# Performance work log

Measured on AMD Instinct MI355X. Metric: run time of the kernel, lower is better.

The kernel has to match this reference:

```python
import jax, jax.numpy as jnp
import numpy as np

N = 200000   # total nodes across batched graphs
E = 800000   # directed edges (grid graph, avg degree ~4)
G = 8        # number of graphs in the batch
IN_DIM, INTER_DIM, OUT_DIM, LAYER_NUM = 2, 128, 64, 4


def setup_inputs() -> dict:
    key = jax.random.key(0)
    ks = jax.random.split(key, 10)
    x = jax.random.normal(ks[0], (N, IN_DIM), jnp.float32)
    edge_index = jax.random.randint(ks[1], (2, E), 0, N, dtype=jnp.int32)
    batch = jnp.sort(jax.random.randint(ks[2], (N,), 0, G, dtype=jnp.int32))

    def glorot(k, fan_in, fan_out):
        s = (2.0 / (fan_in + fan_out)) ** 0.5
        return jax.random.normal(k, (fan_in, fan_out), jnp.float32) * s

    W_in = glorot(ks[3], IN_DIM, INTER_DIM)
    b_in = jnp.zeros((INTER_DIM,), jnp.float32)
    W_hidden = jnp.stack([glorot(jax.random.fold_in(ks[4], i), INTER_DIM, INTER_DIM)
                          for i in range(LAYER_NUM)])
    b_hidden = jnp.zeros((LAYER_NUM, INTER_DIM), jnp.float32)
    W_out = glorot(ks[5], INTER_DIM, OUT_DIM)
    b_out = jnp.zeros((OUT_DIM,), jnp.float32)
    return {"x": x, "edge_index": edge_index, "batch": batch,
            "W_in": W_in, "b_in": b_in, "W_hidden": W_hidden,
            "b_hidden": b_hidden, "W_out": W_out, "b_out": b_out}


def reference(x, edge_index, batch, W_in, b_in, W_hidden, b_hidden, W_out, b_out):
    num_nodes = x.shape[0]
    loops = jnp.arange(num_nodes, dtype=edge_index.dtype)
    # PyG GCNConv: add self loops, symmetric degree normalization
    src = jnp.concatenate([edge_index[0], loops])
    dst = jnp.concatenate([edge_index[1], loops])
    deg = jax.ops.segment_sum(jnp.ones_like(src, x.dtype), dst, num_segments=num_nodes)
    dinv = jnp.where(deg > 0, jax.lax.rsqrt(jnp.maximum(deg, 1.0)), 0.0)
    norm = dinv[src] * dinv[dst]  # [E+N]

    def gcn_conv(h, W, b):
        m = h @ W                                  # [N, F'] dense transform
        msg = norm[:, None] * m[src]               # gather + scale
        out = jax.ops.segment_sum(msg, dst, num_segments=num_nodes)  # scatter-add
        return out + b

    h = gcn_conv(x, W_in, b_in)
    for i in range(W_hidden.shape[0]):
        h = jax.nn.relu(gcn_conv(h, W_hidden[i], b_hidden[i]))
    h = gcn_conv(h, W_out, b_out)

    # global mean pool over batch assignment, then sigmoid
    sums = jax.ops.segment_sum(h, batch, num_segments=G)
    cnts = jax.ops.segment_sum(jnp.ones((num_nodes,), h.dtype), batch, num_segments=G)
    return jax.nn.sigmoid(sums / jnp.maximum(cnts, 1.0)[:, None])
```

## Files before the change

### kernel.cpp

```cpp
#include <hip/hip_runtime.h>
#include <math.h>

#define INTER 128
#define OUTD  64
#define SCAN_T 256
#define SCAN_E 1024
#define NBIN  256
#define PNB2  512
#define NSLOT 64

using bf16x8 = __attribute__((ext_vector_type(8))) short;
using f32x4  = __attribute__((ext_vector_type(4))) float;

static __device__ __forceinline__ unsigned short f2bf(float f) {
    unsigned int u = __float_as_uint(f);
    u += 0x7fffu + ((u >> 16) & 1u);
    return (unsigned short)(u >> 16);
}
static __device__ __forceinline__ unsigned int pk2(float a, float b) {
    return (unsigned int)f2bf(a) | ((unsigned int)f2bf(b) << 16);
}
static __device__ __forceinline__ float bflo(unsigned int u) { return __uint_as_float(u << 16); }
static __device__ __forceinline__ float bfhi(unsigned int u) { return __uint_as_float(u & 0xffff0000u); }

static __device__ __forceinline__ void fma8(float* a, float w, uint4 v) {
    a[0] = fmaf(w, bflo(v.x), a[0]); a[1] = fmaf(w, bfhi(v.x), a[1]);
    a[2] = fmaf(w, bflo(v.y), a[2]); a[3] = fmaf(w, bfhi(v.y), a[3]);
    a[4] = fmaf(w, bflo(v.z), a[4]); a[5] = fmaf(w, bfhi(v.z), a[5]);
    a[6] = fmaf(w, bflo(v.w), a[6]); a[7] = fmaf(w, bfhi(v.w), a[7]);
}
static __device__ __forceinline__ void seed8(float* a, float sn, uint4 v) {
    a[0] = sn * bflo(v.x); a[1] = sn * bfhi(v.x);
    a[2] = sn * bflo(v.y); a[3] = sn * bfhi(v.y);
    a[4] = sn * bflo(v.z); a[5] = sn * bfhi(v.z);
    a[6] = sn * bflo(v.w); a[7] = sn * bfhi(v.w);
}

__global__ void count_k(const int* __restrict__ dst, int* __restrict__ cnt, int E) {
    int e = blockIdx.x * 256 + threadIdx.x;
    if (e < E) atomicAdd(&cnt[dst[e]], 1);
}

__global__ void scan_block(const int* __restrict__ in, int* __restrict__ out,
                           int* __restrict__ bsums, int n) {
    __shared__ int sh[SCAN_T];
    int base = blockIdx.x * SCAN_E;
    int t = threadIdx.x;
    int v[4];
    int s = 0;
#pragma unroll
    for (int i = 0; i < 4; i++) {
        int idx = base + t * 4 + i;
        v[i] = (idx < n) ? in[idx] : 0;
        s += v[i];
    }
    sh[t] = s;
    __syncthreads();
    for (int off = 1; off < SCAN_T; off <<= 1) {
        int x = (t >= off) ? sh[t - off] : 0;
        __syncthreads();
        sh[t] += x;
        __syncthreads();
    }
    int excl = (t == 0) ? 0 : sh[t - 1];
    if (bsums && t == SCAN_T - 1) bsums[blockIdx.x] = sh[t];
#pragma unroll
    for (int i = 0; i < 4; i++) {
        int idx = base + t * 4 + i;
        if (idx < n) out[idx] = excl;
        excl += v[i];
    }
}

__global__ void scan_add(int* __restrict__ out, const int* __restrict__ bsums, int n, int total) {
    int idx = blockIdx.x * SCAN_E + threadIdx.x * 4;
    int add = bsums[blockIdx.x];
#pragma unroll
    for (int i = 0; i < 4; i++) {
        int j = idx + i;
        if (j < n) out[j] += add;
    }
    if (blockIdx.x == 0 && threadIdx.x == 0) out[n] = total;
}

__global__ void scatter_k(const int* __restrict__ src, const int* __restrict__ dst,
                          const int* __restrict__ rs, int* __restrict__ cursor,
                          const float* __restrict__ dinv,
                          int2* __restrict__ cw, int E) {
    int e = blockIdx.x * 256 + threadIdx.x;
    if (e >= E) return;
    int s = src[e], d = dst[e];
    int pos = rs[d] + atomicAdd(&cursor[d], 1);
    cw[pos] = make_int2(s, __float_as_int(dinv[s] * dinv[d]));
}

__global__ __launch_bounds__(256) void prep2_k(const int* __restrict__ cnt,
                                               const int* __restrict__ batch,
                                               float* __restrict__ dinv,
                                               int* __restrict__ blockhist,
                                               int* __restrict__ gstart,
                                               int N, int G, int nblk) {
    __shared__ int hist[NBIN];
    int t = threadIdx.x;
    if (t < NBIN) hist[t] = 0;
    __syncthreads();
    int i = blockIdx.x * 256 + t;
    if (i < N) {
        int d = cnt[i];
        dinv[i] = rsqrtf((float)(d + 1));
        int b = batch[i];
        atomicAdd(&hist[b * 32 + min(d, 31)], 1);
        int prev = (i == 0) ? -1 : batch[i - 1];
        for (int g2 = prev + 1; g2 <= b; g2++) gstart[g2] = i;
        if (i == N - 1) for (int g2 = b + 1; g2 <= G; g2++) gstart[g2] = N;
    }
    __syncthreads();
    if (t < NBIN) blockhist[t * nblk + blockIdx.x] = hist[t];
}

__global__ __launch_bounds__(256) void dorder3_k(const int* __restrict__ cnt,
                                                 const int* __restrict__ batch,
                                                 const int* __restrict__ rs,
                                                 const float* __restrict__ dinv,
                                                 const int* __restrict__ offs,
                                                 int4* __restrict__ srt,
                                                 int N, int nblk) {
    __shared__ int cur[NBIN];
    int t = threadIdx.x;
    if (t < NBIN) cur[t] = 0;
    __syncthreads();
    int i = blockIdx.x * 256 + t;
    if (i >= N) return;
    int key = batch[i] * 32 + min(cnt[i], 31);
    int r = atomicAdd(&cur[key], 1);
    int p = offs[key * nblk + blockIdx.x] + r;
    srt[p] = make_int4(i, rs[i], rs[i + 1], __float_as_int(dinv[i]));
}

__global__ void wprep_h(const float* __restrict__ W, unsigned short* __restrict__ Wt, int L) {
    int tid = blockIdx.x * 256 + threadIdx.x;
    if (tid >= L * INTER * INTER) return;
    int l = tid / (INTER * INTER);
    int r = tid % (INTER * INTER);
    int n = r / INTER, k = r % INTER;
    Wt[tid] = f2bf(W[(size_t)l * INTER * INTER + (size_t)k * INTER + n]);
}

__global__ __launch_bounds__(256) void agg_in_k(const float* __restrict__ x,
                                                const int* __restrict__ rs,
                                                const int2* __restrict__ cw,
                                                const float* __restrict__ dinv,
                                                const float* __restrict__ Wi,
                                                const float* __restrict__ bi,
                                                unsigned short* __restrict__ h, int N) {
    __shared__ float2 axs[256];
    int t = threadIdx.x;
    int i = blockIdx.x * 256 + t;
    float a0 = 0.f, a1 = 0.f;
    if (i < N) {
        float di = dinv[i];
        float sn = di * di;
        float2 xv = ((const float2*)x)[i];
        a0 = sn * xv.x; a1 = sn * xv.y;
        int e0 = rs[i], e1 = rs[i + 1];
        for (int k = e0; k < e1; k += 2) {
            int2 c0 = cw[k];
            int2 c1 = (k + 1 < e1) ? cw[k + 1] : make_int2(0, 0);
            float2 x0 = ((const float2*)x)[c0.x];
            float2 x1 = ((const float2*)x)[c1.x];
            float w0 = __int_as_float(c0.y), w1 = __int_as_float(c1.y);
            a0 = fmaf(w0, x0.x, a0); a1 = fmaf(w0, x0.y, a1);
            a0 = fmaf(w1, x1.x, a0); a1 = fmaf(w1, x1.y, a1);
        }
    }
    axs[t] = make_float2(a0, a1);
    __syncthreads();
    int base = blockIdx.x * 256;
#pragma unroll
    for (int p = 0; p < 16; p++) {
        int nl = p * 16 + (t >> 4);
        int nb = base + nl;
        if (nb < N) {
            int j0 = (t & 15) * 8;
            float2 a = axs[nl];
            float4 wa0 = *(const float4*)&Wi[j0];       float4 wa1 = *(const float4*)&Wi[j0 + 4];
            float4 wb0 = *(const float4*)&Wi[128 + j0]; float4 wb1 = *(const float4*)&Wi[128 + j0 + 4];
            float4 bb0 = *(const float4*)&bi[j0];       float4 bb1 = *(const float4*)&bi[j0 + 4];
            float h0 = fmaf(a.x, wa0.x, fmaf(a.y, wb0.x, bb0.x));
            float h1 = fmaf(a.x, wa0.y, fmaf(a.y, wb0.y, bb0.y));
            float h2 = fmaf(a.x, wa0.z, fmaf(a.y, wb0.z, bb0.z));
            float h3 = fmaf(a.x, wa0.w, fmaf(a.y, wb0.w, bb0.w));
            float h4 = fmaf(a.x, wa1.x, fmaf(a.y, wb1.x, bb1.x));
            float h5 = fmaf(a.x, wa1.y, fmaf(a.y, wb1.y, bb1.y));
            float h6 = fmaf(a.x, wa1.z, fmaf(a.y, wb1.z, bb1.z));
            float h7 = fmaf(a.x, wa1.w, fmaf(a.y, wb1.w, bb1.w));
            *(uint4*)(h + (size_t)nb * 128 + j0) =
                make_uint4(pk2(h0, h1), pk2(h2, h3), pk2(h4, h5), pk2(h6, h7));
        }
    }
}

__global__ __launch_bounds__(256) void fused_hidden7(
    const unsigned short* __restrict__ Hin,
    const int2* __restrict__ cw,
    const int4* __restrict__ srt,
    const unsigned short* __restrict__ Wt,
    const float* __restrict__ bias,
    unsigned short* __restrict__ Hout, int N)
{
    __shared__ __align__(16) unsigned short T[32][136];
    __shared__ int nodeid[32];
    const int t = threadIdx.x;
    const int q = t & 15;
    const int gi = t >> 4;
    const int sA = blockIdx.x * 32 + gi;
    const int sB = sA + 16;
    int4 dA = (sA < N) ? srt[sA] : make_int4(-1, 0, 0, 0);
    int4 dB = (sB < N) ? srt[sB] : make_int4(-1, 0, 0, 0);
    if (q == 0) {
        nodeid[gi]      = dA.x;
        nodeid[gi + 16] = dB.x;
    }

    float accA[8] = {0,0,0,0,0,0,0,0}, accB[8] = {0,0,0,0,0,0,0,0};
    int kA = 0, eA = 0, kB = 0, eB = 0;
    if (dA.x >= 0) {
        float dv = __int_as_float(dA.w);
        seed8(accA, dv * dv, *(const uint4*)(Hin + (size_t)dA.x * 128 + q * 8));
        kA = dA.y; eA = dA.z;
    }
    if (dB.x >= 0) {
        float dv = __int_as_float(dB.w);
        seed8(accB, dv * dv, *(const uint4*)(Hin + (size_t)dB.x * 128 + q * 8));
        kB = dB.y; eB = dB.z;
    }

    while (kA < eA || kB < eB) {
        int2 cA0 = (kA     < eA) ? cw[kA]     : make_int2(0, 0);
        int2 cA1 = (kA + 1 < eA) ? cw[kA + 1] : make_int2(0, 0);
        int2 cA2 = (kA + 2 < eA) ? cw[kA + 2] : make_int2(0, 0);
        int2 cA3 = (kA + 3 < eA) ? cw[kA + 3] : make_int2(0, 0);
        int2 cB0 = (kB     < eB) ? cw[kB]     : make_int2(0, 0);
        int2 cB1 = (kB + 1 < eB) ? cw[kB + 1] : make_int2(0, 0);
        int2 cB2 = (kB + 2 < eB) ? cw[kB + 2] : make_int2(0, 0);
        int2 cB3 = (kB + 3 < eB) ? cw[kB + 3] : make_int2(0, 0);
        uint4 vA0 = *(const uint4*)(Hin + (size_t)cA0.x * 128 + q * 8);
        uint4 vA1 = *(const uint4*)(Hin + (size_t)cA1.x * 128 + q * 8);
        uint4 vA2 = *(const uint4*)(Hin + (size_t)cA2.x * 128 + q * 8);
        uint4 vA3 = *(const uint4*)(Hin + (size_t)cA3.x * 128 + q * 8);
        uint4 vB0 = *(const uint4*)(Hin + (size_t)cB0.x * 128 + q * 8);
        uint4 vB1 = *(const uint4*)(Hin + (size_t)cB1.x * 128 + q * 8);
        uint4 vB2 = *(const uint4*)(Hin + (size_t)cB2.x * 128 + q * 8);
        uint4 vB3 = *(const uint4*)(Hin + (size_t)cB3.x * 128 + q * 8);
        fma8(accA, __int_as_float(cA0.y), vA0);
        fma8(accA, __int_as_float(cA1.y), vA1);
        fma8(accA, __int_as_float(cA2.y), vA2);
        fma8(accA, __int_as_float(cA3.y), vA3);
        fma8(accB, __int_as_float(cB0.y), vB0);
        fma8(accB, __int_as_float(cB1.y), vB1);
        fma8(accB, __int_as_float(cB2.y), vB2);
        fma8(accB, __int_as_float(cB3.y), vB3);
        kA += 4; kB += 4;
    }

    {
        uint4 oA = make_uint4(pk2(accA[0], accA[1]), pk2(accA[2], accA[3]),
                              pk2(accA[4], accA[5]), pk2(accA[6], accA[7]));
        uint4 oB = make_uint4(pk2(accB[0], accB[1]), pk2(accB[2], accB[3]),
                              pk2(accB[4], accB[5]), pk2(accB[6], accB[7]));
        *(uint4*)&T[gi][q * 8] = oA;
        *(uint4*)&T[gi + 16][q * 8] = oB;
    }
    __syncthreads();

    const int wv = t >> 6;
    const int lane = t & 63;
    const int r15 = lane & 15;
    const int kg = lane >> 4;

    bf16x8 bfr[2][4];
#pragma unroll
    for (int nc = 0; nc < 2; nc++)
#pragma unroll
        for (int ks = 0; ks < 4; ks++)
            bfr[nc][ks] = *(const bf16x8*)&T[nc * 16 + r15][kg * 8 + ks * 32];

    f32x4 acc[2][2];
#pragma unroll
    for (int nc = 0; nc < 2; nc++)
#pragma unroll
        for (int c = 0; c < 2; c++) acc[nc][c] = (f32x4){0.f, 0.f, 0.f, 0.f};

#pragma unroll
    for (int c = 0; c < 2; c++) {
        const unsigned short* wrow = Wt + (size_t)(wv * 32 + c * 16 + r15) * 128 + kg * 8;
#pragma unroll
        for (int ks = 0; ks < 4; ks++) {
            bf16x8 afr = *(const bf16x8*)(wrow + ks * 32);
            acc[0][c] = __builtin_amdgcn_mfma_f32_16x16x32_bf16(afr, bfr[0][ks], acc[0][c], 0, 0, 0);
            acc[1][c] = __builtin_amdgcn_mfma_f32_16x16x32_bf16(afr, bfr[1][ks], acc[1][c], 0, 0, 0);
        }
    }

#pragma unroll
    for (int nc = 0; nc < 2; nc++) {
        const int node = nodeid[nc * 16 + r15];
        if (node >= 0) {
#pragma unroll
            for (int c = 0; c < 2; c++) {
                int col = wv * 32 + c * 16 + kg * 4;
                float4 bv = *(const float4*)(bias + col);
                float v0 = fmaxf(acc[nc][c][0] + bv.x, 0.f);
                float v1 = fmaxf(acc[nc][c][1] + bv.y, 0.f);
                float v2 = fmaxf(acc[nc][c][2] + bv.z, 0.f);
                float v3 = fmaxf(acc[nc][c][3] + bv.w, 0.f);
                *(uint2*)(Hout + (size_t)node * 128 + col) = make_uint2(pk2(v0, v1), pk2(v2, v3));
            }
        }
    }
}

__global__ void colsum_k(const int* __restrict__ src, const int* __restrict__ dst,
                         const int* __restrict__ batch, const float* __restrict__ dinv,
                         float* __restrict__ colsum, int N, int E) {
    int e = blockIdx.x * 256 + threadIdx.x;
    if (e < E) {
        int s = src[e], d = dst[e];
        atomicAdd(&colsum[(size_t)batch[d] * N + s], dinv[s] * dinv[d]);
    } else if (e < E + N) {
        int i = e - E;
        float di = dinv[i];
        atomicAdd(&colsum[(size_t)batch[i] * N + i], di * di);
    }
}

__global__ __launch_bounds__(256) void wpool128_k(const unsigned short* __restrict__ hin,
                                                  const float* __restrict__ colsum,
                                                  float* __restrict__ gsum, int N) {
    const int t = threadIdx.x;
    const int wv = t >> 6;
    const int lane = t & 63;
    const int f16 = lane & 15;
    const int r = lane >> 4;
    const int g0 = wv * 2;
    float acc[2][8];
#pragma unroll
    for (int a = 0; a < 2; a++)
#pragma unroll
        for (int b = 0; b < 8; b++) acc[a][b] = 0.f;

    int base = blockIdx.x * PNB2;
    int end = min(base + PNB2, N);
    for (int j = base + r; j < end; j += 4) {
        uint4 v = *(const uint4*)(hin + (size_t)j * 128 + f16 * 8);
        float c0 = colsum[(size_t)g0 * N + j];
        float c1 = colsum[(size_t)(g0 + 1) * N + j];
        float xv[8] = {bflo(v.x), bfhi(v.x), bflo(v.y), bfhi(v.y),
                       bflo(v.z), bfhi(v.z), bflo(v.w), bfhi(v.w)};
#pragma unroll
        for (int b = 0; b < 8; b++) {
            acc[0][b] = fmaf(c0, xv[b], acc[0][b]);
            acc[1][b] = fmaf(c1, xv[b], acc[1][b]);
        }
    }
#pragma unroll
    for (int a = 0; a < 2; a++)
#pragma unroll
        for (int b = 0; b < 8; b++) {
            float v = acc[a][b];
            v += __shfl_xor(v, 16, 64);
            v += __shfl_xor(v, 32, 64);
            acc[a][b] = v;
        }
    if (r == 0) {
        int slot = blockIdx.x & (NSLOT - 1);
        float* dstp = gsum + ((size_t)slot * 8 + g0) * 128 + f16 * 8;
#pragma unroll
        for (int a = 0; a < 2; a++)
#pragma unroll
            for (int b = 0; b < 8; b++)
                atomicAdd(&dstp[(size_t)a * 128 + b], acc[a][b]);
    }
}

__global__ void final6_k(const float* __restrict__ gsum, const int* __restrict__ gstart,
                         const float* __restrict__ W_out, const float* __restrict__ b_out,
                         float* __restrict__ out) {
    __shared__ float sg[8][128];
    int t = threadIdx.x;
    for (int i = t; i < 1024; i += 512) {
        int g = i >> 7, k = i & 127;
        float s = 0.f;
        for (int sl = 0; sl < NSLOT; sl++) s += gsum[((size_t)sl * 8 + g) * 128 + k];
        sg[g][k] = s;
    }
    __syncthreads();
    int g = t / 64, f = t % 64;
    float dot = 0.f;
    for (int k = 0; k < 128; k++) dot = fmaf(sg[g][k], W_out[k * 64 + f], dot);
    int c = gstart[g + 1] - gstart[g];
    float v = dot / (float)max(c, 1) + b_out[f];
    out[g * 64 + f] = 1.f / (1.f + expf(-v));
}

extern "C" void kernel_launch(void* const* d_in, const int* in_sizes, int n_in,
                              void* d_out, int out_size, void* d_ws, size_t ws_size,
                              hipStream_t stream) {
    const float* x     = (const float*)d_in[0];
    const int*   ei    = (const int*)d_in[1];
    const int*   batch = (const int*)d_in[2];
    const float* W_in  = (const float*)d_in[3];
    const float* b_in  = (const float*)d_in[4];
    const float* W_h   = (const float*)d_in[5];
    const float* b_h   = (const float*)d_in[6];
    const float* W_out = (const float*)d_in[7];
    const float* b_out = (const float*)d_in[8];

    const int N = in_sizes[2];
    const int E = in_sizes[1] / 2;
    const int L = in_sizes[5] / (INTER * INTER);
    const int G = 8;
    const int* src = ei;
    const int* dst = ei + E;
    const int nblk = (N + 255) / 256;
    const int nbh = NBIN * nblk;

    char* ws = (char*)d_ws;
    size_t off = 0;
    auto alloc = [&](size_t bytes) -> void* {
        void* p = ws + off;
        off += (bytes + 255) & ~(size_t)255;
        return p;
    };
    int*   cnt    = (int*)alloc((size_t)N * 4);
    int*   cursor = (int*)alloc((size_t)N * 4);
    int*   rs     = (int*)alloc((size_t)(N + 1) * 4);
    int*   bsums  = (int*)alloc(4096);
    float* dinv   = (float*)alloc((size_t)N * 4);
    int2*  cw     = (int2*)alloc((size_t)E * 8);
    unsigned short* h   = (unsigned short*)alloc((size_t)N * INTER * 2);
    unsigned short* h2  = (unsigned short*)alloc((size_t)N * INTER * 2);
    unsigned short* Wht = (unsigned short*)alloc((size_t)L * INTER * INTER * 2);
    float* colsum = (float*)alloc((size_t)8 * N * 4);
    float* gsum   = (float*)alloc((size_t)NSLOT * 8 * 128 * 4);
    int*   gstart = (int*)alloc((G + 1) * 4);
    int*   bh     = (int*)alloc((size_t)(nbh + 1) * 4);
    int4*  srt    = (int4*)alloc((size_t)N * 16);
    (void)ws_size; (void)n_in;

    hipMemsetAsync(cnt, 0, (size_t)N * 8, stream);
    hipMemsetAsync(colsum, 0, (size_t)8 * N * 4, stream);
    hipMemsetAsync(gsum, 0, (size_t)NSLOT * 8 * 128 * 4, stream);

    count_k<<<(E + 255) / 256, 256, 0, stream>>>(dst, cnt, E);
    int nsb = (N + SCAN_E - 1) / SCAN_E;
    scan_block<<<nsb, SCAN_T, 0, stream>>>(cnt, rs, bsums, N);
    scan_block<<<1, SCAN_T, 0, stream>>>(bsums, bsums, nullptr, nsb);
    scan_add<<<nsb, SCAN_T, 0, stream>>>(rs, bsums, N, E);
    prep2_k<<<nblk, 256, 0, stream>>>(cnt, batch, dinv, bh, gstart, N, G, nblk);
    scatter_k<<<(E + 255) / 256, 256, 0, stream>>>(src, dst, rs, cursor, dinv, cw, E);
    colsum_k<<<(E + N + 255) / 256, 256, 0, stream>>>(src, dst, batch, dinv, colsum, N, E);

    int nsb2 = (nbh + SCAN_E - 1) / SCAN_E;
    scan_block<<<nsb2, SCAN_T, 0, stream>>>(bh, bh, bsums, nbh);
    scan_block<<<1, SCAN_T, 0, stream>>>(bsums, bsums, nullptr, nsb2);
    scan_add<<<nsb2, SCAN_T, 0, stream>>>(bh, bsums, nbh, N);
    dorder3_k<<<nblk, 256, 0, stream>>>(cnt, batch, rs, dinv, bh, srt, N, nblk);

    wprep_h<<<(L * INTER * INTER + 255) / 256, 256, 0, stream>>>(W_h, Wht, L);

    agg_in_k<<<nblk, 256, 0, stream>>>(x, rs, cw, dinv, W_in, b_in, h, N);

    unsigned short* hin = h;
    unsigned short* hout = h2;
    for (int l = 0; l < L; l++) {
        fused_hidden7<<<(N + 31) / 32, 256, 0, stream>>>(
            hin, cw, srt, Wht + (size_t)l * INTER * INTER, b_h + (size_t)l * INTER, hout, N);
        unsigned short* tmp = hin; hin = hout; hout = tmp;
    }

    wpool128_k<<<(N + PNB2 - 1) / PNB2, 256, 0, stream>>>(hin, colsum, gsum, N);
    final6_k<<<1, 512, 0, stream>>>(gsum, gstart, W_out, b_out, (float*)d_out);
}
```

Baseline: 521.6 us.

## Use one node per thread-group in hidden layer and fuse scatter with colsum

The hidden-layer kernel now uses 512 threads per block, with each 16-lane group aggregating a single node, unrolled by 8 edges, instead of two interleaved nodes per group. The MFMA stage is split so each of 8 waves produces 16 output columns. Results are staged through shared memory so each node's 256-byte output row is written as one coalesced store. Separately, the CSR scatter and colsum kernels are merged to save a launch and reread inputs once. The tradeoffs are more syncthreads per block, higher register pressure, and per-group load imbalance from the unroll-by-8 padding.

```diff
diff --git a/kernel.cpp b/kernel.cpp
--- a/kernel.cpp
+++ b/kernel.cpp
@@ -83,15 +83,23 @@
     if (blockIdx.x == 0 && threadIdx.x == 0) out[n] = total;
 }
 
-__global__ void scatter_k(const int* __restrict__ src, const int* __restrict__ dst,
-                          const int* __restrict__ rs, int* __restrict__ cursor,
-                          const float* __restrict__ dinv,
-                          int2* __restrict__ cw, int E) {
+__global__ void scatter_cs_k(const int* __restrict__ src, const int* __restrict__ dst,
+                             const int* __restrict__ rs, int* __restrict__ cursor,
+                             const float* __restrict__ dinv, const int* __restrict__ batch,
+                             int2* __restrict__ cw, float* __restrict__ colsum,
+                             int N, int E) {
     int e = blockIdx.x * 256 + threadIdx.x;
-    if (e >= E) return;
-    int s = src[e], d = dst[e];
-    int pos = rs[d] + atomicAdd(&cursor[d], 1);
-    cw[pos] = make_int2(s, __float_as_int(dinv[s] * dinv[d]));
+    if (e < E) {
+        int s = src[e], d = dst[e];
+        float w = dinv[s] * dinv[d];
+        int pos = rs[d] + atomicAdd(&cursor[d], 1);
+        cw[pos] = make_int2(s, __float_as_int(w));
+        atomicAdd(&colsum[(size_t)batch[d] * N + s], w);
+    } else if (e < E + N) {
+        int i = e - E;
+        float di = dinv[i];
+        atomicAdd(&colsum[(size_t)batch[i] * N + i], di * di);
+    }
 }
 
 __global__ __launch_bounds__(256) void prep2_k(const int* __restrict__ cnt,
@@ -200,7 +208,7 @@
     }
 }
 
-__global__ __launch_bounds__(256) void fused_hidden7(
+__global__ __launch_bounds__(512) void fused_hidden9(
     const unsigned short* __restrict__ Hin,
     const int2* __restrict__ cw,
     const int4* __restrict__ srt,
@@ -213,64 +221,34 @@
     const int t = threadIdx.x;
     const int q = t & 15;
     const int gi = t >> 4;
-    const int sA = blockIdx.x * 32 + gi;
-    const int sB = sA + 16;
-    int4 dA = (sA < N) ? srt[sA] : make_int4(-1, 0, 0, 0);
-    int4 dB = (sB < N) ? srt[sB] : make_int4(-1, 0, 0, 0);
-    if (q == 0) {
-        nodeid[gi]      = dA.x;
-        nodeid[gi + 16] = dB.x;
-    }
-
-    float accA[8] = {0,0,0,0,0,0,0,0}, accB[8] = {0,0,0,0,0,0,0,0};
-    int kA = 0, eA = 0, kB = 0, eB = 0;
-    if (dA.x >= 0) {
-        float dv = __int_as_float(dA.w);
-        seed8(accA, dv * dv, *(const uint4*)(Hin + (size_t)dA.x * 128 + q * 8));
-        kA = dA.y; eA = dA.z;
-    }
-    if (dB.x >= 0) {
-        float dv = __int_as_float(dB.w);
-        seed8(accB, dv * dv, *(const uint4*)(Hin + (size_t)dB.x * 128 + q * 8));
-        kB = dB.y; eB = dB.z;
-    }
-
-    while (kA < eA || kB < eB) {
-        int2 cA0 = (kA     < eA) ? cw[kA]     : make_int2(0, 0);
-        int2 cA1 = (kA + 1 < eA) ? cw[kA + 1] : make_int2(0, 0);
-        int2 cA2 = (kA + 2 < eA) ? cw[kA + 2] : make_int2(0, 0);
-        int2 cA3 = (kA + 3 < eA) ? cw[kA + 3] : make_int2(0, 0);
-        int2 cB0 = (kB     < eB) ? cw[kB]     : make_int2(0, 0);
-        int2 cB1 = (kB + 1 < eB) ? cw[kB + 1] : make_int2(0, 0);
-        int2 cB2 = (kB + 2 < eB) ? cw[kB + 2] : make_int2(0, 0);
-        int2 cB3 = (kB + 3 < eB) ? cw[kB + 3] : make_int2(0, 0);
-        uint4 vA0 = *(const uint4*)(Hin + (size_t)cA0.x * 128 + q * 8);
-        uint4 vA1 = *(const uint4*)(Hin + (size_t)cA1.x * 128 + q * 8);
-        uint4 vA2 = *(const uint4*)(Hin + (size_t)cA2.x * 128 + q * 8);
-        uint4 vA3 = *(const uint4*)(Hin + (size_t)cA3.x * 128 + q * 8);
-        uint4 vB0 = *(const uint4*)(Hin + (size_t)cB0.x * 128 + q * 8);
-        uint4 vB1 = *(const uint4*)(Hin + (size_t)cB1.x * 128 + q * 8);
-        uint4 vB2 = *(const uint4*)(Hin + (size_t)cB2.x * 128 + q * 8);
-        uint4 vB3 = *(const uint4*)(Hin + (size_t)cB3.x * 128 + q * 8);
-        fma8(accA, __int_as_float(cA0.y), vA0);
-        fma8(accA, __int_as_float(cA1.y), vA1);
-        fma8(accA, __int_as_float(cA2.y), vA2);
-        fma8(accA, __int_as_float(cA3.y), vA3);
-        fma8(accB, __int_as_float(cB0.y), vB0);
-        fma8(accB, __int_as_float(cB1.y), vB1);
-        fma8(accB, __int_as_float(cB2.y), vB2);
-        fma8(accB, __int_as_float(cB3.y), vB3);
-        kA += 4; kB += 4;
-    }
-
-    {
-        uint4 oA = make_uint4(pk2(accA[0], accA[1]), pk2(accA[2], accA[3]),
-                              pk2(accA[4], accA[5]), pk2(accA[6], accA[7]));
-        uint4 oB = make_uint4(pk2(accB[0], accB[1]), pk2(accB[2], accB[3]),
-                              pk2(accB[4], accB[5]), pk2(accB[6], accB[7]));
-        *(uint4*)&T[gi][q * 8] = oA;
-        *(uint4*)&T[gi + 16][q * 8] = oB;
-    }
+    const int s = blockIdx.x * 32 + gi;
+    int4 d0 = (s < N) ? srt[s] : make_int4(-1, 0, 0, 0);
+    if (q == 0) nodeid[gi] = d0.x;
+
+    float acc[8] = {0,0,0,0,0,0,0,0};
+    int k0 = 0, e0 = 0;
+    if (d0.x >= 0) {
+        float dv = __int_as_float(d0.w);
+        seed8(acc, dv * dv, *(const uint4*)(Hin + (size_t)d0.x * 128 + q * 8));
+        k0 = d0.y; e0 = d0.z;
+    }
+
+    for (int k = k0; k < e0; k += 8) {
+        int2 c[8];
+#pragma unroll
+        for (int u = 0; u < 8; u++)
+            c[u] = (k + u < e0) ? cw[k + u] : make_int2(0, 0);
+        uint4 v[8];
+#pragma unroll
+        for (int u = 0; u < 8; u++)
+            v[u] = *(const uint4*)(Hin + (size_t)c[u].x * 128 + q * 8);
+#pragma unroll
+        for (int u = 0; u < 8; u++)
+            fma8(acc, __int_as_float(c[u].y), v[u]);
+    }
+
+    *(uint4*)&T[gi][q * 8] = make_uint4(pk2(acc[0], acc[1]), pk2(acc[2], acc[3]),
+                                        pk2(acc[4], acc[5]), pk2(acc[6], acc[7]));
     __syncthreads();
 
     const int wv = t >> 6;
@@ -278,59 +256,45 @@
     const int r15 = lane & 15;
     const int kg = lane >> 4;
 
-    bf16x8 bfr[2][4];
-#pragma unroll
-    for (int nc = 0; nc < 2; nc++)
+    bf16x8 wfr[4];
+    {
+        const unsigned short* wrow = Wt + (size_t)(wv * 16 + r15) * 128 + kg * 8;
 #pragma unroll
         for (int ks = 0; ks < 4; ks++)
-            bfr[nc][ks] = *(const bf16x8*)&T[nc * 16 + r15][kg * 8 + ks * 32];
-
-    f32x4 acc[2][2];
-#pragma unroll
-    for (int nc = 0; nc < 2; nc++)
-#pragma unroll
-        for (int c = 0; c < 2; c++) acc[nc][c] = (f32x4){0.f, 0.f, 0.f, 0.f};
-
-#pragma unroll
-    for (int c = 0; c < 2; c++) {
-        const unsigned short* wrow = Wt + (size_t)(wv * 32 + c * 16 + r15) * 128 + kg * 8;
+            wfr[ks] = *(const bf16x8*)(wrow + ks * 32);
+    }
+
+    f32x4 a2[2];
+    a2[0] = (f32x4){0.f, 0.f, 0.f, 0.f};
+    a2[1] = (f32x4){0.f, 0.f, 0.f, 0.f};
+#pragma unroll
+    for (int nc = 0; nc < 2; nc++) {
 #pragma unroll
         for (int ks = 0; ks < 4; ks++) {
-            bf16x8 afr = *(const bf16x8*)(wrow + ks * 32);
-            acc[0][c] = __builtin_amdgcn_mfma_f32_16x16x32_bf16(afr, bfr[0][ks], acc[0][c], 0, 0, 0);
-            acc[1][c] = __builtin_amdgcn_mfma_f32_16x16x32_bf16(afr, bfr[1][ks], acc[1][c], 0, 0, 0);
-        }
-    }
-
-#pragma unroll
-    for (int nc = 0; nc < 2; nc++) {
-        const int node = nodeid[nc * 16 + r15];
-        if (node >= 0) {
-#pragma unroll
-            for (int c = 0; c < 2; c++) {
-                int col = wv * 32 + c * 16 + kg * 4;
-                float4 bv = *(const float4*)(bias + col);
-                float v0 = fmaxf(acc[nc][c][0] + bv.x, 0.f);
-                float v1 = fmaxf(acc[nc][c][1] + bv.y, 0.f);
-                float v2 = fmaxf(acc[nc][c][2] + bv.z, 0.f);
-                float v3 = fmaxf(acc[nc][c][3] + bv.w, 0.f);
-                *(uint2*)(Hout + (size_t)node * 128 + col) = make_uint2(pk2(v0, v1), pk2(v2, v3));
-            }
-        }
-    }
-}
-
-__global__ void colsum_k(const int* __restrict__ src, const int* __restrict__ dst,
-                         const int* __restrict__ batch, const float* __restrict__ dinv,
-                         float* __restrict__ colsum, int N, int E) {
-    int e = blockIdx.x * 256 + threadIdx.x;
-    if (e < E) {
-        int s = src[e], d = dst[e];
-        atomicAdd(&colsum[(size_t)batch[d] * N + s], dinv[s] * dinv[d]);
-    } else if (e < E + N) {
-        int i = e - E;
-        float di = dinv[i];
-        atomicAdd(&colsum[(size_t)batch[i] * N + i], di * di);
+            bf16x8 bfr = *(const bf16x8*)&T[nc * 16 + r15][kg * 8 + ks * 32];
+            a2[nc] = __builtin_amdgcn_mfma_f32_16x16x32_bf16(wfr[ks], bfr, a2[nc], 0, 0, 0);
+        }
+    }
+    __syncthreads();
+
+    {
+        const int col = wv * 16 + kg * 4;
+        const float4 bv = *(const float4*)(bias + col);
+#pragma unroll
+        for (int nc = 0; nc < 2; nc++) {
+            float v0 = fmaxf(a2[nc][0] + bv.x, 0.f);
+            float v1 = fmaxf(a2[nc][1] + bv.y, 0.f);
+            float v2 = fmaxf(a2[nc][2] + bv.z, 0.f);
+            float v3 = fmaxf(a2[nc][3] + bv.w, 0.f);
+            *(uint2*)&T[nc * 16 + r15][col] = make_uint2(pk2(v0, v1), pk2(v2, v3));
+        }
+    }
+    __syncthreads();
+
+    {
+        int node = nodeid[gi];
+        if (node >= 0)
+            *(uint4*)(Hout + (size_t)node * 128 + q * 8) = *(const uint4*)&T[gi][q * 8];
     }
 }
 
@@ -458,8 +422,8 @@
     scan_block<<<1, SCAN_T, 0, stream>>>(bsums, bsums, nullptr, nsb);
     scan_add<<<nsb, SCAN_T, 0, stream>>>(rs, bsums, N, E);
     prep2_k<<<nblk, 256, 0, stream>>>(cnt, batch, dinv, bh, gstart, N, G, nblk);
-    scatter_k<<<(E + 255) / 256, 256, 0, stream>>>(src, dst, rs, cursor, dinv, cw, E);
-    colsum_k<<<(E + N + 255) / 256, 256, 0, stream>>>(src, dst, batch, dinv, colsum, N, E);
+    scatter_cs_k<<<(E + N + 255) / 256, 256, 0, stream>>>(src, dst, rs, cursor, dinv, batch,
+                                                          cw, colsum, N, E);
 
     int nsb2 = (nbh + SCAN_E - 1) / SCAN_E;
     scan_block<<<nsb2, SCAN_T, 0, stream>>>(bh, bh, bsums, nbh);
@@ -474,7 +438,7 @@
     unsigned short* hin = h;
     unsigned short* hout = h2;
     for (int l = 0; l < L; l++) {
-        fused_hidden7<<<(N + 31) / 32, 256, 0, stream>>>(
+        fused_hidden9<<<(N + 31) / 32, 512, 0, stream>>>(
             hin, cw, srt, Wht + (size_t)l * INTER * INTER, b_h + (size_t)l * INTER, hout, N);
         unsigned short* tmp = hin; hin = hout; hout = tmp;
     }
```

Result: no change. 526.5 us (+0.9%).
